# Optimization experiments

Measured on AMD Instinct MI355X. Metric: run time of the kernel, lower is better.

The kernel has to match this reference:

```python
import jax, jax.numpy as jnp
import numpy as np
from jax import lax

DIM = 192
HEADS = 8
B, H, W = 2, 256, 256
EPS = 1e-12  # F.normalize default eps


def conv1x1(x, w):
    # x: [b, ci, h, w], w: [co, ci]
    return jnp.einsum('oi,bihw->bohw', w, x)


def dwconv3x3(x, w):
    # depthwise 3x3, SAME padding; w: [c, 1, 3, 3]
    c = x.shape[1]
    return lax.conv_general_dilated(
        x, w, window_strides=(1, 1), padding='SAME',
        dimension_numbers=('NCHW', 'OIHW', 'NCHW'),
        feature_group_count=c)


def l2norm(x):
    # F.normalize over last axis
    n = jnp.sqrt(jnp.sum(x * x, axis=-1, keepdims=True))
    return x / jnp.maximum(n, EPS)


def setup_inputs() -> dict:
    key = jax.random.key(0)
    ks = jax.random.split(key, 8)
    s = 0.02
    return {
        'x': jax.random.normal(ks[0], (B, DIM, H, W), jnp.float32),
        'x_ref': jax.random.normal(ks[1], (B, DIM, H, W), jnp.float32),
        'wq': jax.random.normal(ks[2], (DIM, DIM), jnp.float32) * s,
        'wq_dw': jax.random.normal(ks[3], (DIM, 1, 3, 3), jnp.float32) * s,
        'wkv': jax.random.normal(ks[4], (2 * DIM, DIM), jnp.float32) * s,
        'wkv_dw': jax.random.normal(ks[5], (2 * DIM, 1, 3, 3), jnp.float32) * s,
        'wproj': jax.random.normal(ks[6], (DIM, DIM), jnp.float32) * s,
        'temperature': jnp.ones((HEADS, 1, 1), jnp.float32),
    }


def reference(x, x_ref, wq, wq_dw, wkv, wkv_dw, wproj, temperature):
    b, c, h, w = x.shape
    ch = c // HEADS  # channels per head
    hw = h * w

    q = dwconv3x3(conv1x1(x, wq), wq_dw)            # [b, c, h, w]
    kv = dwconv3x3(conv1x1(x_ref, wkv), wkv_dw)      # [b, 2c, h, w]
    k, v = jnp.split(kv, 2, axis=1)

    q = q.reshape(b, HEADS, ch, hw)
    k = k.reshape(b, HEADS, ch, hw)
    v = v.reshape(b, HEADS, ch, hw)

    q = l2norm(q)
    k = l2norm(k)

    # channel-wise attention: [b, head, ch, ch]
    attn = jnp.einsum('bhcn,bhdn->bhcd', q, k) * temperature
    attn = jax.nn.softmax(attn, axis=-1)
    out = jnp.einsum('bhcd,bhdn->bhcn', attn, v)     # [b, head, ch, hw]

    out = out.reshape(b, c, h, w)
    out = conv1x1(out, wproj)
    return out
```

## Files before the change

kernel.cpp:

```cpp
#include <hip/hip_runtime.h>
#include <hip/hip_bf16.h>

#define B_ 2
#define C_ 192
#define HEADS_ 8
#define CH_ 24
#define H_ 256
#define W_ 256
#define HW_ 65536


using bf16x8 = __attribute__((ext_vector_type(8))) __bf16;
using f32x4  = __attribute__((ext_vector_type(4))) float;

__device__ __forceinline__ float b2f_us(unsigned short u) {
    return __uint_as_float(((unsigned)u) << 16);
}
__device__ __forceinline__ unsigned short f2bf(float f) {
    union { __hip_bfloat16 b; unsigned short u; } cv;
    cv.b = __float2bfloat16(f);
    return cv.u;
}

__global__ __launch_bounds__(256) void convert_w(
    const float* __restrict__ wq, const float* __restrict__ wkv,
    unsigned short* __restrict__ wqbf, unsigned short* __restrict__ wkvbf)
{
    int i = blockIdx.x * 256 + threadIdx.x;
    const float* src; unsigned short* dst; int qd;
    if (i < 9216) { src = wq;  dst = wqbf;  qd = i; }
    else          { src = wkv; dst = wkvbf; qd = i - 9216; }
    float4 v = *(const float4*)(src + (size_t)qd * 4);
    ushort4 u;
    u.x = f2bf(v.x); u.y = f2bf(v.y); u.z = f2bf(v.z); u.w = f2bf(v.w);
    *(ushort4*)(dst + (size_t)qd * 4) = u;
}

template<bool B_F32, bool OUT_F32>
__global__ __launch_bounds__(256) void gemm_mfma(
    const unsigned short* __restrict__ A, long a_bstride,
    const void* __restrict__ Bv, void* __restrict__ Outv, int outC)
{
    const int nb = blockIdx.x * 64;
    const int mt = blockIdx.y;
    const int b  = blockIdx.z;
    const int t  = threadIdx.x;

    __shared__ unsigned short Al[192 * 40];
    __shared__ unsigned short Bl[64 * 40];

    const unsigned short* Ab = A + (size_t)b * a_bstride + (size_t)mt * 192 * 192;

    const int w = t >> 6, l = t & 63, li = l & 15, q = l >> 4;

    f32x4 acc[3][4];
#pragma unroll
    for (int mi = 0; mi < 3; mi++)
#pragma unroll
        for (int ni = 0; ni < 4; ni++)
            acc[mi][ni] = (f32x4){0.f, 0.f, 0.f, 0.f};

    const int p0 = (t & 15) * 4;
    const int kp = t >> 4;

    for (int kc = 0; kc < 6; kc++) {
        const int k0 = kc * 32;

#pragma unroll
        for (int j = 0; j < 3; j++) {
            int e = t + 256 * j;
            int o = e >> 2, kq = e & 3;
            *(uint4*)&Al[o * 40 + kq * 8] =
                *(const uint4*)(Ab + (size_t)o * 192 + k0 + kq * 8);
        }

        {
            const int k = k0 + kp * 2;
            unsigned int packed[4];
            if (B_F32) {
                const float* Bb = (const float*)Bv + (size_t)b * 192 * HW_;
                float4 r0 = *(const float4*)(Bb + (size_t)k * HW_ + nb + p0);
                float4 r1 = *(const float4*)(Bb + (size_t)(k + 1) * HW_ + nb + p0);
                packed[0] = (unsigned)f2bf(r0.x) | ((unsigned)f2bf(r1.x) << 16);
                packed[1] = (unsigned)f2bf(r0.y) | ((unsigned)f2bf(r1.y) << 16);
                packed[2] = (unsigned)f2bf(r0.z) | ((unsigned)f2bf(r1.z) << 16);
                packed[3] = (unsigned)f2bf(r0.w) | ((unsigned)f2bf(r1.w) << 16);
            } else {
                const unsigned short* Bb = (const unsigned short*)Bv + (size_t)b * 192 * HW_;
                ushort4 r0 = *(const ushort4*)(Bb + (size_t)k * HW_ + nb + p0);
                ushort4 r1 = *(const ushort4*)(Bb + (size_t)(k + 1) * HW_ + nb + p0);
                packed[0] = (unsigned)r0.x | ((unsigned)r1.x << 16);
                packed[1] = (unsigned)r0.y | ((unsigned)r1.y << 16);
                packed[2] = (unsigned)r0.z | ((unsigned)r1.z << 16);
                packed[3] = (unsigned)r0.w | ((unsigned)r1.w << 16);
            }
#pragma unroll
            for (int c = 0; c < 4; c++) {
                int p = p0 + c;
                int rB = ((p & 3) << 4) | (p >> 2);
                *(unsigned int*)&Bl[rB * 40 + kp * 2] = packed[c];
            }
        }
        __syncthreads();

        bf16x8 af[3], bfr[4];
#pragma unroll
        for (int mi = 0; mi < 3; mi++)
            af[mi] = *(const bf16x8*)&Al[(w * 48 + mi * 16 + li) * 40 + q * 8];
#pragma unroll
        for (int ni = 0; ni < 4; ni++)
            bfr[ni] = *(const bf16x8*)&Bl[(ni * 16 + li) * 40 + q * 8];
#pragma unroll
        for (int mi = 0; mi < 3; mi++)
#pragma unroll
            for (int ni = 0; ni < 4; ni++)
                acc[mi][ni] = __builtin_amdgcn_mfma_f32_16x16x32_bf16(
                    af[mi], bfr[ni], acc[mi][ni], 0, 0, 0);
        __syncthreads();
    }

    if (OUT_F32) {
        float* Ob = (float*)Outv + ((size_t)b * outC + (size_t)mt * 192) * HW_;
#pragma unroll
        for (int mi = 0; mi < 3; mi++)
#pragma unroll
            for (int r = 0; r < 4; r++) {
                int o = w * 48 + mi * 16 + q * 4 + r;
                float4 vv;
                vv.x = acc[mi][0][r]; vv.y = acc[mi][1][r];
                vv.z = acc[mi][2][r]; vv.w = acc[mi][3][r];
                *(float4*)(Ob + (size_t)o * HW_ + nb + 4 * li) = vv;
            }
    } else {
        unsigned short* Ob = (unsigned short*)Outv + ((size_t)b * outC + (size_t)mt * 192) * HW_;
#pragma unroll
        for (int mi = 0; mi < 3; mi++)
#pragma unroll
            for (int r = 0; r < 4; r++) {
                int o = w * 48 + mi * 16 + q * 4 + r;
                ushort4 u;
                u.x = f2bf(acc[mi][0][r]); u.y = f2bf(acc[mi][1][r]);
                u.z = f2bf(acc[mi][2][r]); u.w = f2bf(acc[mi][3][r]);
                *(ushort4*)(Ob + (size_t)o * HW_ + nb + 4 * li) = u;
            }
    }
}

__global__ __launch_bounds__(256) void dwconv_v(
    const __hip_bfloat16* __restrict__ tmpKV, const float* __restrict__ wkv_dw,
    __hip_bfloat16* __restrict__ V)
{
    const int y = blockIdx.x, cg = blockIdx.y, b = blockIdx.z;
    const int t = threadIdx.x;
    const int c = cg * 32 + (t >> 3);
    const int x0 = (t & 7) * 32;
    const unsigned short* base =
        (const unsigned short*)(tmpKV + ((size_t)b * 2 * C_ + C_ + c) * HW_);
    const float* wp = wkv_dw + (size_t)(C_ + c) * 9;
    float wgt[9];
#pragma unroll
    for (int i = 0; i < 9; i++) wgt[i] = wp[i];

    float o[32];
#pragma unroll
    for (int i = 0; i < 32; i++) o[i] = 0.f;

#pragma unroll
    for (int dy = -1; dy <= 1; dy++) {
        int yy = y + dy;
        if ((unsigned)yy >= 256u) continue;
        const unsigned short* r = base + yy * W_;
        float v[34];
        v[0]  = (x0 > 0) ? b2f_us(r[x0 - 1]) : 0.f;
        v[33] = (x0 + 32 < 256) ? b2f_us(r[x0 + 32]) : 0.f;
        const uint4* r4 = (const uint4*)(r + x0);
#pragma unroll
        for (int m = 0; m < 4; m++) {
            uint4 raw = r4[m];
            unsigned u;
            u = raw.x; v[1 + 8*m + 0] = __uint_as_float(u << 16); v[1 + 8*m + 1] = __uint_as_float(u & 0xffff0000u);
            u = raw.y; v[1 + 8*m + 2] = __uint_as_float(u << 16); v[1 + 8*m + 3] = __uint_as_float(u & 0xffff0000u);
            u = raw.z; v[1 + 8*m + 4] = __uint_as_float(u << 16); v[1 + 8*m + 5] = __uint_as_float(u & 0xffff0000u);
            u = raw.w; v[1 + 8*m + 6] = __uint_as_float(u << 16); v[1 + 8*m + 7] = __uint_as_float(u & 0xffff0000u);
        }
        float w0 = wgt[3 * (dy + 1) + 0];
        float w1 = wgt[3 * (dy + 1) + 1];
        float w2 = wgt[3 * (dy + 1) + 2];
#pragma unroll
        for (int i = 0; i < 32; i++)
            o[i] += v[i] * w0 + v[i + 1] * w1 + v[i + 2] * w2;
    }
    unsigned short* dst = (unsigned short*)V + ((size_t)b * C_ + c) * HW_ + y * W_ + x0;
#pragma unroll
    for (int m = 0; m < 4; m++) {
        uint4 pk;
        pk.x = (unsigned)f2bf(o[8*m + 0]) | ((unsigned)f2bf(o[8*m + 1]) << 16);
        pk.y = (unsigned)f2bf(o[8*m + 2]) | ((unsigned)f2bf(o[8*m + 3]) << 16);
        pk.z = (unsigned)f2bf(o[8*m + 4]) | ((unsigned)f2bf(o[8*m + 5]) << 16);
        pk.w = (unsigned)f2bf(o[8*m + 6]) | ((unsigned)f2bf(o[8*m + 7]) << 16);
        *(uint4*)(dst + 8 * m) = pk;
    }
}

#define PADB 264
#define YG 4
__global__ __launch_bounds__(256) void dw_qk_gram(
    const __hip_bfloat16* __restrict__ tmpQ,
    const __hip_bfloat16* __restrict__ tmpKV,
    const float* __restrict__ wq_dw, const float* __restrict__ wkv_dw,
    float* __restrict__ G, float* __restrict__ sq, float* __restrict__ sk)
{
    const int y0 = blockIdx.x * YG, h = blockIdx.y, b = blockIdx.z;
    const int t = threadIdx.x;

    __shared__ unsigned short Qs[CH_ * PADB];
    __shared__ unsigned short Ks[CH_ * PADB];
    __shared__ float sqs[CH_], sks[CH_];

    if (t < CH_) { sqs[t] = 0.f; sks[t] = 0.f; }

    const int w = t >> 6, l = t & 63, li = l & 15, q = l >> 4;
    const int tr = w >> 1, tc = w & 1;
    int ar = tr * 16 + li; if (ar > 23) ar = 23;
    int br = tc * 16 + li; if (br > 23) br = 23;
    const unsigned short* arow = &Qs[ar * PADB];
    const unsigned short* brow = &Ks[br * PADB];
    f32x4 acc = (f32x4){0.f, 0.f, 0.f, 0.f};

    __syncthreads();

    for (int yi = 0; yi < YG; yi++) {
        const int y = y0 + yi;

        for (int u = t; u < 384; u += 256) {
            const int tens = (u >= 192);
            const int rem = u - tens * 192;
            const int c = rem >> 3;
            const int x0 = (rem & 7) * 32;
            const unsigned short* base = tens
                ? (const unsigned short*)(tmpKV + ((size_t)b * 2 * C_ + h * CH_ + c) * HW_)
                : (const unsigned short*)(tmpQ  + ((size_t)b * C_     + h * CH_ + c) * HW_);
            const float* wp = (tens ? wkv_dw : wq_dw) + (size_t)(h * CH_ + c) * 9;

            float o[32];
#pragma unroll
            for (int i = 0; i < 32; i++) o[i] = 0.f;

#pragma unroll
            for (int dy = -1; dy <= 1; dy++) {
                int yy = y + dy;
                if ((unsigned)yy >= 256u) continue;
                const unsigned short* r = base + yy * W_;
                float v[34];
                v[0]  = (x0 > 0) ? b2f_us(r[x0 - 1]) : 0.f;
                v[33] = (x0 + 32 < 256) ? b2f_us(r[x0 + 32]) : 0.f;
                const uint4* r4 = (const uint4*)(r + x0);
#pragma unroll
                for (int m = 0; m < 4; m++) {
                    uint4 raw = r4[m];
                    unsigned uu;
                    uu = raw.x; v[1 + 8*m + 0] = __uint_as_float(uu << 16); v[1 + 8*m + 1] = __uint_as_float(uu & 0xffff0000u);
                    uu = raw.y; v[1 + 8*m + 2] = __uint_as_float(uu << 16); v[1 + 8*m + 3] = __uint_as_float(uu & 0xffff0000u);
                    uu = raw.z; v[1 + 8*m + 4] = __uint_as_float(uu << 16); v[1 + 8*m + 5] = __uint_as_float(uu & 0xffff0000u);
                    uu = raw.w; v[1 + 8*m + 6] = __uint_as_float(uu << 16); v[1 + 8*m + 7] = __uint_as_float(uu & 0xffff0000u);
                }
                float w0 = wp[3 * (dy + 1) + 0];
                float w1 = wp[3 * (dy + 1) + 1];
                float w2 = wp[3 * (dy + 1) + 2];
#pragma unroll
                for (int i = 0; i < 32; i++)
                    o[i] += v[i] * w0 + v[i + 1] * w1 + v[i + 2] * w2;
            }

            float s = 0.f;
#pragma unroll
            for (int i = 0; i < 32; i++) s += o[i] * o[i];
            atomicAdd(tens ? &sks[c] : &sqs[c], s);

            unsigned short* dst = (tens ? Ks : Qs) + c * PADB + x0;
#pragma unroll
            for (int m = 0; m < 4; m++) {
                uint4 pk;
                pk.x = (unsigned)f2bf(o[8*m + 0]) | ((unsigned)f2bf(o[8*m + 1]) << 16);
                pk.y = (unsigned)f2bf(o[8*m + 2]) | ((unsigned)f2bf(o[8*m + 3]) << 16);
                pk.z = (unsigned)f2bf(o[8*m + 4]) | ((unsigned)f2bf(o[8*m + 5]) << 16);
                pk.w = (unsigned)f2bf(o[8*m + 6]) | ((unsigned)f2bf(o[8*m + 7]) << 16);
                *(uint4*)(dst + 8 * m) = pk;
            }
        }
        __syncthreads();

#pragma unroll
        for (int ks = 0; ks < 8; ks++) {
            bf16x8 af = *(const bf16x8*)&arow[ks * 32 + q * 8];
            bf16x8 bf = *(const bf16x8*)&brow[ks * 32 + q * 8];
            acc = __builtin_amdgcn_mfma_f32_16x16x32_bf16(af, bf, acc, 0, 0, 0);
        }
        __syncthreads();
    }

    if (t < CH_) {
        atomicAdd(&sq[b * C_ + h * CH_ + t], sqs[t]);
        atomicAdd(&sk[b * C_ + h * CH_ + t], sks[t]);
    }

    float* Gb = G + (size_t)(b * HEADS_ + h) * CH_ * CH_;
    const int col = tc * 16 + li;
    if (col < CH_) {
#pragma unroll
        for (int r = 0; r < 4; r++) {
            int row = tr * 16 + q * 4 + r;
            if (row < CH_)
                atomicAdd(&Gb[row * CH_ + col], acc[r]);
        }
    }
}

__global__ __launch_bounds__(192) void softmax_proj(
    const float* __restrict__ G, const float* __restrict__ sq,
    const float* __restrict__ sk, const float* __restrict__ temperature,
    const float* __restrict__ wproj, unsigned short* __restrict__ Mbf)
{
    const int h = blockIdx.x, b = blockIdx.y, t = threadIdx.x;
    __shared__ float attn[CH_][CH_];
    __shared__ float rk[CH_];
    const float* Gb = G + (size_t)(b * HEADS_ + h) * CH_ * CH_;
    if (t < CH_)
        rk[t] = 1.f / fmaxf(sqrtf(sk[b * C_ + h * CH_ + t]), 1e-12f);
    __syncthreads();
    if (t < CH_) {
        float rq = 1.f / fmaxf(sqrtf(sq[b * C_ + h * CH_ + t]), 1e-12f);
        float tempv = temperature[h];
        float row[CH_];
        float mx = -1e30f;
        for (int d = 0; d < CH_; d++) {
            row[d] = Gb[t * CH_ + d] * rq * rk[d] * tempv;
            mx = fmaxf(mx, row[d]);
        }
        float s = 0.f;
        for (int d = 0; d < CH_; d++) { row[d] = __expf(row[d] - mx); s += row[d]; }
        float inv = 1.f / s;
        for (int d = 0; d < CH_; d++) attn[t][d] = row[d] * inv;
    }
    __syncthreads();
    const int o = t;
    float wrow[CH_];
    for (int c = 0; c < CH_; c++) wrow[c] = wproj[o * C_ + h * CH_ + c];
    for (int d = 0; d < CH_; d++) {
        float s = 0.f;
        for (int c = 0; c < CH_; c++) s += wrow[c] * attn[c][d];
        Mbf[((size_t)b * C_ + o) * C_ + h * CH_ + d] = f2bf(s);
    }
}

extern "C" void kernel_launch(void* const* d_in, const int* in_sizes, int n_in,
                              void* d_out, int out_size, void* d_ws, size_t ws_size,
                              hipStream_t stream)
{
    const float* x           = (const float*)d_in[0];
    const float* x_ref       = (const float*)d_in[1];
    const float* wq          = (const float*)d_in[2];
    const float* wq_dw       = (const float*)d_in[3];
    const float* wkv         = (const float*)d_in[4];
    const float* wkv_dw      = (const float*)d_in[5];
    const float* wproj       = (const float*)d_in[6];
    const float* temperature = (const float*)d_in[7];
    float* out = (float*)d_out;

    char* ws = (char*)d_ws;
    __hip_bfloat16* tmpQ  = (__hip_bfloat16*)(ws);
    __hip_bfloat16* tmpKV = (__hip_bfloat16*)(ws + 50331648);
    __hip_bfloat16* tmpV  = (__hip_bfloat16*)(ws);
    float* G  = (float*)(ws + 150994944);
    float* sq = (float*)(ws + 151031808);
    float* sk = (float*)(ws + 151033344);
    unsigned short* wqbf  = (unsigned short*)(ws + 151034880);
    unsigned short* wkvbf = (unsigned short*)(ws + 151108608);
    unsigned short* Mbf   = (unsigned short*)(ws + 151034880);

    hipMemsetAsync(G, 0, 36864 + 1536 + 1536, stream);

    convert_w<<<dim3(108), 256, 0, stream>>>(wq, wkv, wqbf, wkvbf);
    gemm_mfma<true, false><<<dim3(HW_ / 64, 1, B_), 256, 0, stream>>>(
        wqbf, 0, x, tmpQ, 192);
    gemm_mfma<true, false><<<dim3(HW_ / 64, 2, B_), 256, 0, stream>>>(
        wkvbf, 0, x_ref, tmpKV, 384);
    dw_qk_gram<<<dim3(H_ / YG, HEADS_, B_), 256, 0, stream>>>(
        tmpQ, tmpKV, wq_dw, wkv_dw, G, sq, sk);
    softmax_proj<<<dim3(HEADS_, B_), 192, 0, stream>>>(
        G, sq, sk, temperature, wproj, Mbf);
    dwconv_v<<<dim3(H_, 6, B_), 256, 0, stream>>>(tmpKV, wkv_dw, tmpV);
    gemm_mfma<false, true><<<dim3(HW_ / 64, 1, B_), 256, 0, stream>>>(
        Mbf, 192 * 192, tmpV, out, 192);
}
```

Baseline: 434.6 us.

## Stage full-K B tile once in LDS, read A from global, batch dwconv rows

The GEMM kernel now loads the whole 192-deep B tile into LDS in one pass with a single barrier, instead of six K-chunks that each needed two barriers. The A weight fragments are read directly from global memory (L2-resident) rather than staged through LDS. This removes barriers and the A LDS traffic, but makes each MFMA wait on global loads. The V depthwise conv also processes four rows per block, cutting block count and reusing weight loads, at the cost of fewer blocks in flight.

```diff
diff --git a/kernel.cpp b/kernel.cpp
--- a/kernel.cpp
+++ b/kernel.cpp
@@ -36,6 +36,7 @@
     *(ushort4*)(dst + (size_t)qd * 4) = u;
 }
 
+#define BPITCH 200
 template<bool B_F32, bool OUT_F32>
 __global__ __launch_bounds__(256) void gemm_mfma(
     const unsigned short* __restrict__ A, long a_bstride,
@@ -46,8 +47,7 @@
     const int b  = blockIdx.z;
     const int t  = threadIdx.x;
 
-    __shared__ unsigned short Al[192 * 40];
-    __shared__ unsigned short Bl[64 * 40];
+    __shared__ unsigned short Bl[64 * BPITCH];
 
     const unsigned short* Ab = A + (size_t)b * a_bstride + (size_t)mt * 192 * 192;
 
@@ -63,60 +63,52 @@
     const int p0 = (t & 15) * 4;
     const int kp = t >> 4;
 
+#pragma unroll
     for (int kc = 0; kc < 6; kc++) {
-        const int k0 = kc * 32;
-
-#pragma unroll
-        for (int j = 0; j < 3; j++) {
-            int e = t + 256 * j;
-            int o = e >> 2, kq = e & 3;
-            *(uint4*)&Al[o * 40 + kq * 8] =
-                *(const uint4*)(Ab + (size_t)o * 192 + k0 + kq * 8);
-        }
-
-        {
-            const int k = k0 + kp * 2;
-            unsigned int packed[4];
-            if (B_F32) {
-                const float* Bb = (const float*)Bv + (size_t)b * 192 * HW_;
-                float4 r0 = *(const float4*)(Bb + (size_t)k * HW_ + nb + p0);
-                float4 r1 = *(const float4*)(Bb + (size_t)(k + 1) * HW_ + nb + p0);
-                packed[0] = (unsigned)f2bf(r0.x) | ((unsigned)f2bf(r1.x) << 16);
-                packed[1] = (unsigned)f2bf(r0.y) | ((unsigned)f2bf(r1.y) << 16);
-                packed[2] = (unsigned)f2bf(r0.z) | ((unsigned)f2bf(r1.z) << 16);
-                packed[3] = (unsigned)f2bf(r0.w) | ((unsigned)f2bf(r1.w) << 16);
-            } else {
-                const unsigned short* Bb = (const unsigned short*)Bv + (size_t)b * 192 * HW_;
-                ushort4 r0 = *(const ushort4*)(Bb + (size_t)k * HW_ + nb + p0);
-                ushort4 r1 = *(const ushort4*)(Bb + (size_t)(k + 1) * HW_ + nb + p0);
-                packed[0] = (unsigned)r0.x | ((unsigned)r1.x << 16);
-                packed[1] = (unsigned)r0.y | ((unsigned)r1.y << 16);
-                packed[2] = (unsigned)r0.z | ((unsigned)r1.z << 16);
-                packed[3] = (unsigned)r0.w | ((unsigned)r1.w << 16);
-            }
-#pragma unroll
-            for (int c = 0; c < 4; c++) {
-                int p = p0 + c;
-                int rB = ((p & 3) << 4) | (p >> 2);
-                *(unsigned int*)&Bl[rB * 40 + kp * 2] = packed[c];
-            }
-        }
-        __syncthreads();
-
+        const int k = kc * 32 + kp * 2;
+        unsigned int packed[4];
+        if (B_F32) {
+            const float* Bb = (const float*)Bv + (size_t)b * 192 * HW_;
+            float4 r0 = *(const float4*)(Bb + (size_t)k * HW_ + nb + p0);
+            float4 r1 = *(const float4*)(Bb + (size_t)(k + 1) * HW_ + nb + p0);
+            packed[0] = (unsigned)f2bf(r0.x) | ((unsigned)f2bf(r1.x) << 16);
+            packed[1] = (unsigned)f2bf(r0.y) | ((unsigned)f2bf(r1.y) << 16);
+            packed[2] = (unsigned)f2bf(r0.z) | ((unsigned)f2bf(r1.z) << 16);
+            packed[3] = (unsigned)f2bf(r0.w) | ((unsigned)f2bf(r1.w) << 16);
+        } else {
+            const unsigned short* Bb = (const unsigned short*)Bv + (size_t)b * 192 * HW_;
+            ushort4 r0 = *(const ushort4*)(Bb + (size_t)k * HW_ + nb + p0);
+            ushort4 r1 = *(const ushort4*)(Bb + (size_t)(k + 1) * HW_ + nb + p0);
+            packed[0] = (unsigned)r0.x | ((unsigned)r1.x << 16);
+            packed[1] = (unsigned)r0.y | ((unsigned)r1.y << 16);
+            packed[2] = (unsigned)r0.z | ((unsigned)r1.z << 16);
+            packed[3] = (unsigned)r0.w | ((unsigned)r1.w << 16);
+        }
+#pragma unroll
+        for (int c = 0; c < 4; c++) {
+            int p = p0 + c;
+            int rB = ((p & 3) << 4) | (p >> 2);
+            *(unsigned int*)&Bl[rB * BPITCH + k] = packed[c];
+        }
+    }
+    __syncthreads();
+
+#pragma unroll
+    for (int kc = 0; kc < 6; kc++) {
         bf16x8 af[3], bfr[4];
 #pragma unroll
         for (int mi = 0; mi < 3; mi++)
-            af[mi] = *(const bf16x8*)&Al[(w * 48 + mi * 16 + li) * 40 + q * 8];
+            af[mi] = *(const bf16x8*)(Ab + (size_t)(w * 48 + mi * 16 + li) * 192
+                                         + kc * 32 + q * 8);
 #pragma unroll
         for (int ni = 0; ni < 4; ni++)
-            bfr[ni] = *(const bf16x8*)&Bl[(ni * 16 + li) * 40 + q * 8];
+            bfr[ni] = *(const bf16x8*)&Bl[(ni * 16 + li) * BPITCH + kc * 32 + q * 8];
 #pragma unroll
         for (int mi = 0; mi < 3; mi++)
 #pragma unroll
             for (int ni = 0; ni < 4; ni++)
                 acc[mi][ni] = __builtin_amdgcn_mfma_f32_16x16x32_bf16(
                     af[mi], bfr[ni], acc[mi][ni], 0, 0, 0);
-        __syncthreads();
     }
 
     if (OUT_F32) {
@@ -146,11 +138,12 @@
     }
 }
 
+#define VYG 4
 __global__ __launch_bounds__(256) void dwconv_v(
     const __hip_bfloat16* __restrict__ tmpKV, const float* __restrict__ wkv_dw,
     __hip_bfloat16* __restrict__ V)
 {
-    const int y = blockIdx.x, cg = blockIdx.y, b = blockIdx.z;
+    const int y0 = blockIdx.x * VYG, cg = blockIdx.y, b = blockIdx.z;
     const int t = threadIdx.x;
     const int c = cg * 32 + (t >> 3);
     const int x0 = (t & 7) * 32;
@@ -161,44 +154,47 @@
 #pragma unroll
     for (int i = 0; i < 9; i++) wgt[i] = wp[i];
 
-    float o[32];
-#pragma unroll
-    for (int i = 0; i < 32; i++) o[i] = 0.f;
-
-#pragma unroll
-    for (int dy = -1; dy <= 1; dy++) {
-        int yy = y + dy;
-        if ((unsigned)yy >= 256u) continue;
-        const unsigned short* r = base + yy * W_;
-        float v[34];
-        v[0]  = (x0 > 0) ? b2f_us(r[x0 - 1]) : 0.f;
-        v[33] = (x0 + 32 < 256) ? b2f_us(r[x0 + 32]) : 0.f;
-        const uint4* r4 = (const uint4*)(r + x0);
+    for (int yi = 0; yi < VYG; yi++) {
+        const int y = y0 + yi;
+        float o[32];
+#pragma unroll
+        for (int i = 0; i < 32; i++) o[i] = 0.f;
+
+#pragma unroll
+        for (int dy = -1; dy <= 1; dy++) {
+            int yy = y + dy;
+            if ((unsigned)yy >= 256u) continue;
+            const unsigned short* r = base + yy * W_;
+            float v[34];
+            v[0]  = (x0 > 0) ? b2f_us(r[x0 - 1]) : 0.f;
+            v[33] = (x0 + 32 < 256) ? b2f_us(r[x0 + 32]) : 0.f;
+            const uint4* r4 = (const uint4*)(r + x0);
+#pragma unroll
+            for (int m = 0; m < 4; m++) {
+                uint4 raw = r4[m];
+                unsigned u;
+                u = raw.x; v[1 + 8*m + 0] = __uint_as_float(u << 16); v[1 + 8*m + 1] = __uint_as_float(u & 0xffff0000u);
+                u = raw.y; v[1 + 8*m + 2] = __uint_as_float(u << 16); v[1 + 8*m + 3] = __uint_as_float(u & 0xffff0000u);
+                u = raw.z; v[1 + 8*m + 4] = __uint_as_float(u << 16); v[1 + 8*m + 5] = __uint_as_float(u & 0xffff0000u);
+                u = raw.w; v[1 + 8*m + 6] = __uint_as_float(u << 16); v[1 + 8*m + 7] = __uint_as_float(u & 0xffff0000u);
+            }
+            float w0 = wgt[3 * (dy + 1) + 0];
+            float w1 = wgt[3 * (dy + 1) + 1];
+            float w2 = wgt[3 * (dy + 1) + 2];
+#pragma unroll
+            for (int i = 0; i < 32; i++)
+                o[i] += v[i] * w0 + v[i + 1] * w1 + v[i + 2] * w2;
+        }
+        unsigned short* dst = (unsigned short*)V + ((size_t)b * C_ + c) * HW_ + y * W_ + x0;
 #pragma unroll
         for (int m = 0; m < 4; m++) {
-            uint4 raw = r4[m];
-            unsigned u;
-            u = raw.x; v[1 + 8*m + 0] = __uint_as_float(u << 16); v[1 + 8*m + 1] = __uint_as_float(u & 0xffff0000u);
-            u = raw.y; v[1 + 8*m + 2] = __uint_as_float(u << 16); v[1 + 8*m + 3] = __uint_as_float(u & 0xffff0000u);
-            u = raw.z; v[1 + 8*m + 4] = __uint_as_float(u << 16); v[1 + 8*m + 5] = __uint_as_float(u & 0xffff0000u);
-            u = raw.w; v[1 + 8*m + 6] = __uint_as_float(u << 16); v[1 + 8*m + 7] = __uint_as_float(u & 0xffff0000u);
-        }
-        float w0 = wgt[3 * (dy + 1) + 0];
-        float w1 = wgt[3 * (dy + 1) + 1];
-        float w2 = wgt[3 * (dy + 1) + 2];
-#pragma unroll
-        for (int i = 0; i < 32; i++)
-            o[i] += v[i] * w0 + v[i + 1] * w1 + v[i + 2] * w2;
-    }
-    unsigned short* dst = (unsigned short*)V + ((size_t)b * C_ + c) * HW_ + y * W_ + x0;
-#pragma unroll
-    for (int m = 0; m < 4; m++) {
-        uint4 pk;
-        pk.x = (unsigned)f2bf(o[8*m + 0]) | ((unsigned)f2bf(o[8*m + 1]) << 16);
-        pk.y = (unsigned)f2bf(o[8*m + 2]) | ((unsigned)f2bf(o[8*m + 3]) << 16);
-        pk.z = (unsigned)f2bf(o[8*m + 4]) | ((unsigned)f2bf(o[8*m + 5]) << 16);
-        pk.w = (unsigned)f2bf(o[8*m + 6]) | ((unsigned)f2bf(o[8*m + 7]) << 16);
-        *(uint4*)(dst + 8 * m) = pk;
+            uint4 pk;
+            pk.x = (unsigned)f2bf(o[8*m + 0]) | ((unsigned)f2bf(o[8*m + 1]) << 16);
+            pk.y = (unsigned)f2bf(o[8*m + 2]) | ((unsigned)f2bf(o[8*m + 3]) << 16);
+            pk.z = (unsigned)f2bf(o[8*m + 4]) | ((unsigned)f2bf(o[8*m + 5]) << 16);
+            pk.w = (unsigned)f2bf(o[8*m + 6]) | ((unsigned)f2bf(o[8*m + 7]) << 16);
+            *(uint4*)(dst + 8 * m) = pk;
+        }
     }
 }
 
@@ -389,7 +385,7 @@
         tmpQ, tmpKV, wq_dw, wkv_dw, G, sq, sk);
     softmax_proj<<<dim3(HEADS_, B_), 192, 0, stream>>>(
         G, sq, sk, temperature, wproj, Mbf);
-    dwconv_v<<<dim3(H_, 6, B_), 256, 0, stream>>>(tmpKV, wkv_dw, tmpV);
+    dwconv_v<<<dim3(H_ / VYG, 6, B_), 256, 0, stream>>>(tmpKV, wkv_dw, tmpV);
     gemm_mfma<false, true><<<dim3(HW_ / 64, 1, B_), 256, 0, stream>>>(
         Mbf, 192 * 192, tmpV, out, 192);
 }
```

Result: slower. 447.0 us (+2.9%).
